# Kernel tuning notes

Hardware: AMD Instinct MI355X
Metric: run time of the kernel (lower is better)

## Reference

```python
import jax, jax.numpy as jnp
import numpy as np

N_NODES = 100000
N_EDGES = 1600000
NUM_FEATURES = 128
HIDDEN = 128


def _linear_init(key, fan_in, fan_out):
    kw, kb = jax.random.split(key)
    bound = 1.0 / np.sqrt(fan_in)
    w = jax.random.uniform(kw, (fan_in, fan_out), jnp.float32, -bound, bound)
    b = jax.random.uniform(kb, (fan_out,), jnp.float32, -bound, bound)
    return w, b


def setup_inputs() -> dict:
    key = jax.random.key(0)
    ks = jax.random.split(key, 8)
    x = jax.random.normal(ks[0], (N_NODES, NUM_FEATURES), jnp.float32)
    edge_index = jax.random.randint(ks[1], (2, N_EDGES), 0, N_NODES, jnp.int64)
    w11, b11 = _linear_init(ks[2], NUM_FEATURES, HIDDEN)
    w12, b12 = _linear_init(ks[3], HIDDEN, HIDDEN)
    w21, b21 = _linear_init(ks[4], HIDDEN, HIDDEN)
    w22, b22 = _linear_init(ks[5], HIDDEN, HIDDEN)
    w31, b31 = _linear_init(ks[6], HIDDEN, HIDDEN)
    w32, b32 = _linear_init(ks[7], HIDDEN, 1)
    return {"x": x, "edge_index": edge_index,
            "w11": w11, "b11": b11, "w12": w12, "b12": b12,
            "w21": w21, "b21": b21, "w22": w22, "b22": b22,
            "w31": w31, "b31": b31, "w32": w32, "b32": b32}


def _gin_conv(x, src, dst, w1, b1, w2, b2):
    # GINConv (eps=0): h_i = MLP(x_i + sum_{j->i} x_j)
    agg = jax.ops.segment_sum(x[src], dst, num_segments=N_NODES)
    h = x + agg
    h = jax.nn.relu(h @ w1 + b1)
    return h @ w2 + b2


def reference(x, edge_index, w11, b11, w12, b12, w21, b21, w22, b22, w31, b31, w32, b32):
    src, dst = edge_index[0], edge_index[1]
    h = _gin_conv(x, src, dst, w11, b11, w12, b12)
    h = _gin_conv(h, src, dst, w21, b21, w22, b22)
    h = _gin_conv(h, src, dst, w31, b31, w32, b32)  # [N, 1]
    return h
```

## Files before the change

kernel.cpp:

```cpp
#include <hip/hip_runtime.h>

#define NN 100000
#define NE 1600000
#define F 128
#define HALFN 50000
#define NBUCK ((NN + 255) >> 8)
#define SCAT_BLOCKS 512
#define EPB (NE / SCAT_BLOCKS)
#define TROWS 64
#define NTILE ((NN + TROWS - 1) / TROWS)
#define IDX_CAP 1536

typedef _Float16 f16x8 __attribute__((ext_vector_type(8)));
typedef float    f32x4 __attribute__((ext_vector_type(4)));
typedef unsigned short ushort8v __attribute__((ext_vector_type(8)));
typedef unsigned short ushort4v __attribute__((ext_vector_type(4)));

__device__ inline unsigned short f2h(float f) {
    _Float16 h = (_Float16)f;
    return __builtin_bit_cast(unsigned short, h);
}
__device__ inline float h2f(unsigned short u) {
    return (float)__builtin_bit_cast(_Float16, u);
}

__global__ __launch_bounds__(256) void k_bhist(const int* __restrict__ dst, int* __restrict__ bcnt) {
    __shared__ int sc[NBUCK];
    for (int i = threadIdx.x; i < NBUCK; i += 256) sc[i] = 0;
    __syncthreads();
    int stride = gridDim.x * 256;
    for (int e = blockIdx.x * 256 + threadIdx.x; e < NE; e += stride)
        atomicAdd(&sc[dst[e] >> 8], 1);
    __syncthreads();
    for (int i = threadIdx.x; i < NBUCK; i += 256) {
        int c = sc[i];
        if (c) atomicAdd(&bcnt[i], c);
    }
}

__global__ void k_bscan(const int* __restrict__ bcnt, int* __restrict__ bbase, int* __restrict__ bcur) {
    __shared__ int s[512];
    int t = threadIdx.x;
    int v = (t < NBUCK) ? bcnt[t] : 0;
    s[t] = v;
    __syncthreads();
    for (int off = 1; off < 512; off <<= 1) {
        int u = (t >= off) ? s[t - off] : 0;
        __syncthreads();
        s[t] += u;
        __syncthreads();
    }
    int excl = s[t] - v;
    if (t < NBUCK) { bbase[t] = excl; bcur[t] = excl; }
    if (t == 0) bbase[NBUCK] = NE;
}

__global__ __launch_bounds__(256) void k_scatterA(const int* __restrict__ src,
                                                  const int* __restrict__ dst,
                                                  int* __restrict__ bcur,
                                                  unsigned* __restrict__ scratch) {
    __shared__ uint2 sEdge[EPB];
    __shared__ int cnt[512];
    __shared__ int scn[512];
    __shared__ int cntB[512];
    __shared__ int gbase[512];
    __shared__ int ssum[256];

    const int tid = threadIdx.x;
    const int ebase = blockIdx.x * EPB;

#pragma unroll
    for (int i = tid; i < 512; i += 256) { cnt[i] = 0; cntB[i] = 0; }
    __syncthreads();

    for (int i = tid; i < EPB; i += 256) {
        int b = dst[ebase + i] >> 8;
        atomicAdd(&cnt[b], 1);
    }
    __syncthreads();

    int c0 = cnt[2 * tid], c1 = cnt[2 * tid + 1];
    ssum[tid] = c0 + c1;
    __syncthreads();
    for (int off = 1; off < 256; off <<= 1) {
        int v = (tid >= off) ? ssum[tid - off] : 0;
        __syncthreads();
        ssum[tid] += v;
        __syncthreads();
    }
    int texcl = (tid == 0) ? 0 : ssum[tid - 1];
    scn[2 * tid] = texcl;
    scn[2 * tid + 1] = texcl + c0;
#pragma unroll
    for (int i = tid; i < NBUCK; i += 256) {
        int c = cnt[i];
        gbase[i] = c ? atomicAdd(&bcur[i], c) : 0;
    }
    __syncthreads();

    for (int i = tid; i < EPB; i += 256) {
        int s = src[ebase + i], d = dst[ebase + i];
        int b = d >> 8;
        int rank = atomicAdd(&cntB[b], 1);
        sEdge[scn[b] + rank] = make_uint2((unsigned)s, (unsigned)d);
    }
    __syncthreads();

    for (int i = tid; i < EPB; i += 256) {
        uint2 ed = sEdge[i];
        int b = (int)(ed.y >> 8);
        unsigned w = ((ed.y & 255u) << 24) | ed.x;
        scratch[gbase[b] + (i - scn[b])] = w;
    }
}

__global__ __launch_bounds__(256) void k_fillB(const int* __restrict__ bbase,
                                               const unsigned* __restrict__ scratch,
                                               int* __restrict__ row_ptr,
                                               int* __restrict__ csr) {
    __shared__ int cnt[256];
    __shared__ int s[256];
    __shared__ int cur[256];
    int b = blockIdx.x;
    int base = bbase[b], end = bbase[b + 1];
    int t = threadIdx.x;
    cnt[t] = 0;
    __syncthreads();
    for (int i = base + t; i < end; i += 256)
        atomicAdd(&cnt[scratch[i] >> 24], 1);
    __syncthreads();
    int v = cnt[t];
    s[t] = v;
    __syncthreads();
    for (int off = 1; off < 256; off <<= 1) {
        int u = (t >= off) ? s[t - off] : 0;
        __syncthreads();
        s[t] += u;
        __syncthreads();
    }
    int excl = s[t] - v;
    int node = (b << 8) + t;
    if (node < NN) row_ptr[node] = base + excl;
    if (b == NBUCK - 1 && t == 0) row_ptr[NN] = NE;
    cur[t] = excl;
    __syncthreads();
    for (int i = base + t; i < end; i += 256) {
        unsigned w = scratch[i];
        int n = w >> 24;
        int p = atomicAdd(&cur[n], 1);
        csr[base + p] = (int)(w & 0xFFFFFFu);
    }
}

__global__ __launch_bounds__(256) void k_x2h(const float* __restrict__ x, unsigned short* __restrict__ xh) {
    int j = blockIdx.x * 256 + threadIdx.x;
    int c = blockIdx.y;
    if (j >= NN) return;
    const float4* px = (const float4*)&x[(size_t)j * F + c * 32];
    unsigned short* o = &xh[((size_t)c * NN + j) * 32];
#pragma unroll
    for (int half = 0; half < 4; ++half) {
        float4 v0 = px[half * 2], v1 = px[half * 2 + 1];
        ushort8v h;
        h[0] = f2h(v0.x); h[1] = f2h(v0.y); h[2] = f2h(v0.z); h[3] = f2h(v0.w);
        h[4] = f2h(v1.x); h[5] = f2h(v1.y); h[6] = f2h(v1.z); h[7] = f2h(v1.w);
        *(ushort8v*)(o + half * 8) = h;
    }
}

struct WPack {
    const float* w[5];
    unsigned short* t[5];
};

__global__ void k_w2h(WPack p) {
    int which = blockIdx.x >> 6;
    int idx = (blockIdx.x & 63) * 256 + threadIdx.x;
    int n = idx >> 7, k = idx & 127;
    p.t[which][idx] = f2h(p.w[which][k * 128 + n]);
}

template <bool LOC>
__device__ __forceinline__ void accum_half(float a[8], int st, int e,
                                           const int* __restrict__ sIdx,
                                           const int* __restrict__ gIdx,
                                           const unsigned short* __restrict__ Gc,
                                           int lofs, bool hb) {
    int p = st;
    for (; p + 4 <= e; p += 4) {
        int j0 = LOC ? sIdx[p]     : gIdx[p];
        int j1 = LOC ? sIdx[p + 1] : gIdx[p + 1];
        int j2 = LOC ? sIdx[p + 2] : gIdx[p + 2];
        int j3 = LOC ? sIdx[p + 3] : gIdx[p + 3];
        ushort8v v0 = {}, v1 = {}, v2 = {}, v3 = {};
        if ((j0 >= HALFN) == hb) v0 = *(const ushort8v*)&Gc[(size_t)j0 * 32 + lofs];
        if ((j1 >= HALFN) == hb) v1 = *(const ushort8v*)&Gc[(size_t)j1 * 32 + lofs];
        if ((j2 >= HALFN) == hb) v2 = *(const ushort8v*)&Gc[(size_t)j2 * 32 + lofs];
        if ((j3 >= HALFN) == hb) v3 = *(const ushort8v*)&Gc[(size_t)j3 * 32 + lofs];
#pragma unroll
        for (int k = 0; k < 8; ++k)
            a[k] += (h2f(v0[k]) + h2f(v1[k])) + (h2f(v2[k]) + h2f(v3[k]));
    }
    for (; p < e; ++p) {
        int j0 = LOC ? sIdx[p] : gIdx[p];
        if ((j0 >= HALFN) == hb) {
            ushort8v v0 = *(const ushort8v*)&Gc[(size_t)j0 * 32 + lofs];
#pragma unroll
            for (int k = 0; k < 8; ++k) a[k] += h2f(v0[k]);
        }
    }
}

__global__ __launch_bounds__(256, 8) void k_agg(const unsigned short* __restrict__ G,
                                                const int* __restrict__ row_ptr,
                                                const int* __restrict__ csr,
                                                unsigned short* __restrict__ PART) {
    __shared__ int sRP[TROWS + 1];
    __shared__ int sIdx[IDX_CAP];

    const int tid  = threadIdx.x;
    const int tile = blockIdx.x >> 3;
    const int cc   = blockIdx.x & 7;
    const int c    = cc & 3;
    const bool hb  = (cc >> 2) != 0;
    const int row0 = tile * TROWS;
    const unsigned short* Gc = G + (size_t)c * NN * 32;

    if (tid < TROWS + 1) {
        int n = row0 + tid;
        if (n > NN) n = NN;
        sRP[tid] = row_ptr[n];
    }
    __syncthreads();
    const int ibase = sRP[0];
    const int icnt  = sRP[TROWS] - ibase;
    const int icap  = icnt < IDX_CAP ? icnt : IDX_CAP;
    for (int i = tid; i < icap; i += 256) sIdx[i] = csr[ibase + i];
    __syncthreads();

    const int g    = tid >> 2;
    const int lofs = (tid & 3) * 8;
    const int node = row0 + g;
    if (node >= NN) return;

    float a[8] = {};
    if ((node >= HALFN) == hb) {
        ushort8v sh = *(const ushort8v*)&Gc[(size_t)node * 32 + lofs];
#pragma unroll
        for (int k = 0; k < 8; ++k) a[k] = h2f(sh[k]);
    }

    int st = sRP[g] - ibase, e = sRP[g + 1] - ibase;
    if (e <= icap)
        accum_half<true>(a, st, e, sIdx, csr + ibase, Gc, lofs, hb);
    else
        accum_half<false>(a, st, e, sIdx, csr + ibase, Gc, lofs, hb);

    ushort8v o;
#pragma unroll
    for (int k = 0; k < 8; ++k) o[k] = f2h(a[k]);
    *(ushort8v*)&PART[((size_t)cc * NN + node) * 32 + lofs] = o;
}

template <int L3>
__global__ __launch_bounds__(256, 6) void k_mlp(const unsigned short* __restrict__ PART,
                                                const unsigned short* __restrict__ W1,
                                                const float* __restrict__ b1,
                                                const unsigned short* __restrict__ W2,
                                                const float* __restrict__ b2,
                                                const float* __restrict__ w32,
                                                const float* __restrict__ b32,
                                                unsigned short* __restrict__ H,
                                                float* __restrict__ out) {
    __shared__ __align__(16) unsigned short sA[64 * 128];

    const int tid = threadIdx.x;
    const int row0 = blockIdx.x * 64;
    const int cg   = tid >> 6;
    const int lane = tid & 63;
    const int m16  = lane & 15;
    const int quad = lane >> 4;
    const size_t H1OFF = (size_t)4 * NN * 32;

#pragma unroll
    for (int i = 0; i < 4; ++i) {
        int unit = i * 256 + tid;
        int c    = unit >> 8;
        int idx  = unit & 255;
        int node = idx >> 2;
        int q    = idx & 3;
        ushort8v o = {};
        if (row0 + node < NN) {
            size_t base = ((size_t)c * NN + row0 + node) * 32 + q * 8;
            ushort8v v0 = *(const ushort8v*)&PART[base];
            ushort8v v1 = *(const ushort8v*)&PART[H1OFF + base];
#pragma unroll
            for (int k = 0; k < 8; ++k) o[k] = f2h(h2f(v0[k]) + h2f(v1[k]));
        }
        int u = c * 4 + q;
        *(ushort8v*)&sA[node * 128 + ((u ^ (node & 15)) << 3)] = o;
    }
    __syncthreads();

    f32x4 acc[4][2] = {};
#pragma unroll
    for (int ks = 0; ks < 4; ++ks) {
        f16x8 a[4];
#pragma unroll
        for (int rt = 0; rt < 4; ++rt) {
            int rowL = rt * 16 + m16;
            int u = ks * 4 + quad;
            a[rt] = *(const f16x8*)&sA[rowL * 128 + ((u ^ (rowL & 15)) << 3)];
        }
#pragma unroll
        for (int ct = 0; ct < 2; ++ct) {
            int widx = (cg * 32 + ct * 16 + m16) * 128 + ks * 32 + quad * 8;
            f16x8 b = *(const f16x8*)&W1[widx];
#pragma unroll
            for (int rt = 0; rt < 4; ++rt)
                acc[rt][ct] = __builtin_amdgcn_mfma_f32_16x16x32_f16(a[rt], b, acc[rt][ct], 0, 0, 0);
        }
    }

    if (L3) {
        float* psf = (float*)sA;
        __syncthreads();
#pragma unroll
        for (int rt = 0; rt < 4; ++rt) {
            float s[4] = {0.f, 0.f, 0.f, 0.f};
#pragma unroll
            for (int ct = 0; ct < 2; ++ct) {
                int col = cg * 32 + ct * 16 + m16;
                float bv = b1[col];
                float wv = w32[col];
#pragma unroll
                for (int i = 0; i < 4; ++i) {
                    float v = fmaxf(acc[rt][ct][i] + bv, 0.f);
                    s[i] += v * wv;
                }
            }
#pragma unroll
            for (int i = 0; i < 4; ++i) {
#pragma unroll
                for (int mask = 1; mask < 16; mask <<= 1)
                    s[i] += __shfl_xor(s[i], mask, 64);
            }
            if (m16 == 0) {
#pragma unroll
                for (int i = 0; i < 4; ++i) {
                    int rowL = rt * 16 + quad * 4 + i;
                    psf[rowL * 4 + cg] = s[i];
                }
            }
        }
        __syncthreads();
        if (tid < 64) {
            int row = row0 + tid;
            if (row < NN)
                out[row] = (psf[tid * 4] + psf[tid * 4 + 1]) + (psf[tid * 4 + 2] + psf[tid * 4 + 3]) + b32[0];
        }
        return;
    }

    __syncthreads();
#pragma unroll
    for (int rt = 0; rt < 4; ++rt) {
#pragma unroll
        for (int ct = 0; ct < 2; ++ct) {
            int col = cg * 32 + ct * 16 + m16;
            float bv = b1[col];
#pragma unroll
            for (int i = 0; i < 4; ++i) {
                int rL = rt * 16 + quad * 4 + i;
                float v = fmaxf(acc[rt][ct][i] + bv, 0.f);
                sA[rL * 128 + (((col >> 3) ^ (rL & 15)) << 3) + (col & 7)] = f2h(v);
            }
        }
    }
    __syncthreads();

    f32x4 acc2[4][2] = {};
#pragma unroll
    for (int ks = 0; ks < 4; ++ks) {
        f16x8 a[4];
#pragma unroll
        for (int rt = 0; rt < 4; ++rt) {
            int rowL = rt * 16 + m16;
            int u = ks * 4 + quad;
            a[rt] = *(const f16x8*)&sA[rowL * 128 + ((u ^ (rowL & 15)) << 3)];
        }
#pragma unroll
        for (int ct = 0; ct < 2; ++ct) {
            int widx = (cg * 32 + ct * 16 + m16) * 128 + ks * 32 + quad * 8;
            f16x8 b = *(const f16x8*)&W2[widx];
#pragma unroll
            for (int rt = 0; rt < 4; ++rt)
                acc2[rt][ct] = __builtin_amdgcn_mfma_f32_16x16x32_f16(a[rt], b, acc2[rt][ct], 0, 0, 0);
        }
    }

    __syncthreads();
#pragma unroll
    for (int rt = 0; rt < 4; ++rt) {
#pragma unroll
        for (int ct = 0; ct < 2; ++ct) {
            int col = cg * 32 + ct * 16 + m16;
            float bv = b2[col];
#pragma unroll
            for (int i = 0; i < 4; ++i) {
                int rL = rt * 16 + quad * 4 + i;
                float v = acc2[rt][ct][i] + bv;
                sA[rL * 128 + (((col >> 3) ^ (rL & 15)) << 3) + (col & 7)] = f2h(v);
            }
        }
    }
    __syncthreads();
    {
#pragma unroll
        for (int i = 0; i < 4; ++i) {
            int unit = i * 256 + tid;
            int c    = unit >> 8;
            int idx  = unit & 255;
            int node = idx >> 2;
            int q    = idx & 3;
            int u    = c * 4 + q;
            if (row0 + node < NN)
                *(ushort8v*)&H[((size_t)c * NN + row0 + node) * 32 + q * 8] =
                    *(const ushort8v*)&sA[node * 128 + ((u ^ (node & 15)) << 3)];
        }
    }
}

static inline size_t align256(size_t x) { return (x + 255) & ~(size_t)255; }

extern "C" void kernel_launch(void* const* d_in, const int* in_sizes, int n_in,
                              void* d_out, int out_size, void* d_ws, size_t ws_size,
                              hipStream_t stream) {
    const float* x   = (const float*)d_in[0];
    const int*   ei  = (const int*)d_in[1];
    const float* w11 = (const float*)d_in[2];
    const float* b11 = (const float*)d_in[3];
    const float* w12 = (const float*)d_in[4];
    const float* b12 = (const float*)d_in[5];
    const float* w21 = (const float*)d_in[6];
    const float* b21 = (const float*)d_in[7];
    const float* w22 = (const float*)d_in[8];
    const float* b22 = (const float*)d_in[9];
    const float* w31 = (const float*)d_in[10];
    const float* b31 = (const float*)d_in[11];
    const float* w32 = (const float*)d_in[12];
    const float* b32 = (const float*)d_in[13];
    float* out = (float*)d_out;

    const int* src = ei;
    const int* dst = ei + NE;

    char* ws = (char*)d_ws;
    size_t off = 0;
    unsigned short* Abuf = (unsigned short*)(ws + off); off += align256((size_t)NN * F * 2);
    unsigned short* Bbuf = (unsigned short*)(ws + off); off += align256((size_t)NN * F * 2);
    unsigned short* PART = (unsigned short*)(ws + off); off += align256((size_t)NN * F * 2 * 2);
    int* bcnt    = (int*)(ws + off); off += align256((size_t)NBUCK * 4);
    int* bbase   = (int*)(ws + off); off += align256((size_t)(NBUCK + 1) * 4);
    int* bcur    = (int*)(ws + off); off += align256((size_t)NBUCK * 4);
    int* row_ptr = (int*)(ws + off); off += align256((size_t)(NN + 1) * 4);
    int* csr     = (int*)(ws + off); off += align256((size_t)NE * 4);
    unsigned* scratch = (unsigned*)(ws + off); off += align256((size_t)NE * 4);
    unsigned short* wt[5];
    for (int i = 0; i < 5; ++i) {
        wt[i] = (unsigned short*)(ws + off); off += align256((size_t)128 * 128 * 2);
    }
    (void)ws_size;

    WPack wp;
    wp.w[0] = w11; wp.w[1] = w12; wp.w[2] = w21; wp.w[3] = w22; wp.w[4] = w31;
    for (int i = 0; i < 5; ++i) wp.t[i] = wt[i];
    k_w2h<<<320, 256, 0, stream>>>(wp);
    {
        dim3 gx((NN + 255) / 256, 4);
        k_x2h<<<gx, 256, 0, stream>>>(x, Abuf);
    }

    (void)hipMemsetAsync(bcnt, 0, (size_t)NBUCK * 4, stream);
    k_bhist<<<512, 256, 0, stream>>>(dst, bcnt);
    k_bscan<<<1, 512, 0, stream>>>(bcnt, bbase, bcur);
    k_scatterA<<<SCAT_BLOCKS, 256, 0, stream>>>(src, dst, bcur, scratch);
    k_fillB<<<NBUCK, 256, 0, stream>>>(bbase, scratch, row_ptr, csr);

    const int mlpTiles = (NN + 63) / 64;
    const int aggBlocks = NTILE * 8;

    k_agg<<<aggBlocks, 256, 0, stream>>>(Abuf, row_ptr, csr, PART);
    k_mlp<0><<<mlpTiles, 256, 0, stream>>>(PART, wt[0], b11, wt[1], b12,
                                           nullptr, nullptr, Bbuf, nullptr);
    k_agg<<<aggBlocks, 256, 0, stream>>>(Bbuf, row_ptr, csr, PART);
    k_mlp<0><<<mlpTiles, 256, 0, stream>>>(PART, wt[2], b21, wt[3], b22,
                                           nullptr, nullptr, Abuf, nullptr);
    k_agg<<<aggBlocks, 256, 0, stream>>>(Abuf, row_ptr, csr, PART);
    k_mlp<1><<<mlpTiles, 256, 0, stream>>>(PART, wt[4], b31, nullptr, nullptr,
                                           w32, b32, nullptr, out);
}
```

Measured before the change: 464.3 us.

## Partition CSR neighbor lists by source half so aggregation skips filtering

The CSR build now sorts each node's neighbor list into two groups, sources below and at-or-above the half-node boundary, and records a per-node split pointer. Each aggregation block, which handles one half of the source nodes, then walks only its own sub-range and loads neighbors unconditionally. Before, every block scanned the whole list and branched per index. This cuts the index reads and divergent predicated loads in the three aggregation passes. In exchange the CSR build does a bit more work and one extra row_split array is stored and read.

Result: faster. 432.9 us (-6.8%).

```diff
diff --git a/kernel.cpp b/kernel.cpp
--- a/kernel.cpp
+++ b/kernel.cpp
@@ -117,38 +117,49 @@
 __global__ __launch_bounds__(256) void k_fillB(const int* __restrict__ bbase,
                                                const unsigned* __restrict__ scratch,
                                                int* __restrict__ row_ptr,
+                                               int* __restrict__ row_split,
                                                int* __restrict__ csr) {
-    __shared__ int cnt[256];
-    __shared__ int s[256];
-    __shared__ int cur[256];
+    __shared__ int cnt[512];
+    __shared__ int cur[512];
+    __shared__ int ssum[256];
     int b = blockIdx.x;
     int base = bbase[b], end = bbase[b + 1];
     int t = threadIdx.x;
-    cnt[t] = 0;
-    __syncthreads();
-    for (int i = base + t; i < end; i += 256)
-        atomicAdd(&cnt[scratch[i] >> 24], 1);
-    __syncthreads();
-    int v = cnt[t];
-    s[t] = v;
-    __syncthreads();
-    for (int off = 1; off < 256; off <<= 1) {
-        int u = (t >= off) ? s[t - off] : 0;
-        __syncthreads();
-        s[t] += u;
-        __syncthreads();
-    }
-    int excl = s[t] - v;
-    int node = (b << 8) + t;
-    if (node < NN) row_ptr[node] = base + excl;
-    if (b == NBUCK - 1 && t == 0) row_ptr[NN] = NE;
-    cur[t] = excl;
+    cnt[t] = 0; cnt[t + 256] = 0;
     __syncthreads();
     for (int i = base + t; i < end; i += 256) {
         unsigned w = scratch[i];
         int n = w >> 24;
-        int p = atomicAdd(&cur[n], 1);
-        csr[base + p] = (int)(w & 0xFFFFFFu);
+        int h = (int)((w & 0xFFFFFFu) >= HALFN);
+        atomicAdd(&cnt[n * 2 + h], 1);
+    }
+    __syncthreads();
+    int c0 = cnt[2 * t], c1 = cnt[2 * t + 1];
+    ssum[t] = c0 + c1;
+    __syncthreads();
+    for (int off = 1; off < 256; off <<= 1) {
+        int u = (t >= off) ? ssum[t - off] : 0;
+        __syncthreads();
+        ssum[t] += u;
+        __syncthreads();
+    }
+    int texcl = (t == 0) ? 0 : ssum[t - 1];
+    int node = (b << 8) + t;
+    if (node < NN) {
+        row_ptr[node]   = base + texcl;
+        row_split[node] = base + texcl + c0;
+    }
+    if (b == NBUCK - 1 && t == 0) row_ptr[NN] = NE;
+    cur[2 * t] = texcl;
+    cur[2 * t + 1] = texcl + c0;
+    __syncthreads();
+    for (int i = base + t; i < end; i += 256) {
+        unsigned w = scratch[i];
+        int n = w >> 24;
+        int srcv = (int)(w & 0xFFFFFFu);
+        int h = (int)(srcv >= HALFN);
+        int p = atomicAdd(&cur[n * 2 + h], 1);
+        csr[base + p] = srcv;
     }
 }
 
@@ -181,48 +192,47 @@
 }
 
 template <bool LOC>
-__device__ __forceinline__ void accum_half(float a[8], int st, int e,
-                                           const int* __restrict__ sIdx,
-                                           const int* __restrict__ gIdx,
-                                           const unsigned short* __restrict__ Gc,
-                                           int lofs, bool hb) {
+__device__ __forceinline__ void accum1(float a[8], int st, int e,
+                                       const int* __restrict__ sIdx,
+                                       const int* __restrict__ gIdx,
+                                       const unsigned short* __restrict__ Gc,
+                                       int lofs) {
     int p = st;
     for (; p + 4 <= e; p += 4) {
         int j0 = LOC ? sIdx[p]     : gIdx[p];
         int j1 = LOC ? sIdx[p + 1] : gIdx[p + 1];
         int j2 = LOC ? sIdx[p + 2] : gIdx[p + 2];
         int j3 = LOC ? sIdx[p + 3] : gIdx[p + 3];
-        ushort8v v0 = {}, v1 = {}, v2 = {}, v3 = {};
-        if ((j0 >= HALFN) == hb) v0 = *(const ushort8v*)&Gc[(size_t)j0 * 32 + lofs];
-        if ((j1 >= HALFN) == hb) v1 = *(const ushort8v*)&Gc[(size_t)j1 * 32 + lofs];
-        if ((j2 >= HALFN) == hb) v2 = *(const ushort8v*)&Gc[(size_t)j2 * 32 + lofs];
-        if ((j3 >= HALFN) == hb) v3 = *(const ushort8v*)&Gc[(size_t)j3 * 32 + lofs];
+        ushort8v v0 = *(const ushort8v*)&Gc[(size_t)j0 * 32 + lofs];
+        ushort8v v1 = *(const ushort8v*)&Gc[(size_t)j1 * 32 + lofs];
+        ushort8v v2 = *(const ushort8v*)&Gc[(size_t)j2 * 32 + lofs];
+        ushort8v v3 = *(const ushort8v*)&Gc[(size_t)j3 * 32 + lofs];
 #pragma unroll
         for (int k = 0; k < 8; ++k)
             a[k] += (h2f(v0[k]) + h2f(v1[k])) + (h2f(v2[k]) + h2f(v3[k]));
     }
     for (; p < e; ++p) {
         int j0 = LOC ? sIdx[p] : gIdx[p];
-        if ((j0 >= HALFN) == hb) {
-            ushort8v v0 = *(const ushort8v*)&Gc[(size_t)j0 * 32 + lofs];
-#pragma unroll
-            for (int k = 0; k < 8; ++k) a[k] += h2f(v0[k]);
-        }
+        ushort8v v0 = *(const ushort8v*)&Gc[(size_t)j0 * 32 + lofs];
+#pragma unroll
+        for (int k = 0; k < 8; ++k) a[k] += h2f(v0[k]);
     }
 }
 
 __global__ __launch_bounds__(256, 8) void k_agg(const unsigned short* __restrict__ G,
                                                 const int* __restrict__ row_ptr,
+                                                const int* __restrict__ row_split,
                                                 const int* __restrict__ csr,
                                                 unsigned short* __restrict__ PART) {
     __shared__ int sRP[TROWS + 1];
+    __shared__ int sSP[TROWS];
     __shared__ int sIdx[IDX_CAP];
 
     const int tid  = threadIdx.x;
     const int tile = blockIdx.x >> 3;
     const int cc   = blockIdx.x & 7;
     const int c    = cc & 3;
-    const bool hb  = (cc >> 2) != 0;
+    const int hb   = cc >> 2;
     const int row0 = tile * TROWS;
     const unsigned short* Gc = G + (size_t)c * NN * 32;
 
@@ -230,6 +240,9 @@
         int n = row0 + tid;
         if (n > NN) n = NN;
         sRP[tid] = row_ptr[n];
+    } else if (tid >= 128 && tid < 128 + TROWS) {
+        int n = row0 + (tid - 128);
+        sSP[tid - 128] = (n < NN) ? row_split[n] : NE;
     }
     __syncthreads();
     const int ibase = sRP[0];
@@ -244,17 +257,19 @@
     if (node >= NN) return;
 
     float a[8] = {};
-    if ((node >= HALFN) == hb) {
+    if ((node >= HALFN) == (hb != 0)) {
         ushort8v sh = *(const ushort8v*)&Gc[(size_t)node * 32 + lofs];
 #pragma unroll
         for (int k = 0; k < 8; ++k) a[k] = h2f(sh[k]);
     }
 
-    int st = sRP[g] - ibase, e = sRP[g + 1] - ibase;
+    int st, e;
+    if (hb == 0) { st = sRP[g] - ibase; e = sSP[g] - ibase; }
+    else         { st = sSP[g] - ibase; e = sRP[g + 1] - ibase; }
     if (e <= icap)
-        accum_half<true>(a, st, e, sIdx, csr + ibase, Gc, lofs, hb);
+        accum1<true>(a, st, e, sIdx, csr + ibase, Gc, lofs);
     else
-        accum_half<false>(a, st, e, sIdx, csr + ibase, Gc, lofs, hb);
+        accum1<false>(a, st, e, sIdx, csr + ibase, Gc, lofs);
 
     ushort8v o;
 #pragma unroll
@@ -460,11 +475,12 @@
     unsigned short* Abuf = (unsigned short*)(ws + off); off += align256((size_t)NN * F * 2);
     unsigned short* Bbuf = (unsigned short*)(ws + off); off += align256((size_t)NN * F * 2);
     unsigned short* PART = (unsigned short*)(ws + off); off += align256((size_t)NN * F * 2 * 2);
-    int* bcnt    = (int*)(ws + off); off += align256((size_t)NBUCK * 4);
-    int* bbase   = (int*)(ws + off); off += align256((size_t)(NBUCK + 1) * 4);
-    int* bcur    = (int*)(ws + off); off += align256((size_t)NBUCK * 4);
-    int* row_ptr = (int*)(ws + off); off += align256((size_t)(NN + 1) * 4);
-    int* csr     = (int*)(ws + off); off += align256((size_t)NE * 4);
+    int* bcnt      = (int*)(ws + off); off += align256((size_t)NBUCK * 4);
+    int* bbase     = (int*)(ws + off); off += align256((size_t)(NBUCK + 1) * 4);
+    int* bcur      = (int*)(ws + off); off += align256((size_t)NBUCK * 4);
+    int* row_ptr   = (int*)(ws + off); off += align256((size_t)(NN + 1) * 4);
+    int* row_split = (int*)(ws + off); off += align256((size_t)NN * 4);
+    int* csr       = (int*)(ws + off); off += align256((size_t)NE * 4);
     unsigned* scratch = (unsigned*)(ws + off); off += align256((size_t)NE * 4);
     unsigned short* wt[5];
     for (int i = 0; i < 5; ++i) {
@@ -485,18 +501,18 @@
     k_bhist<<<512, 256, 0, stream>>>(dst, bcnt);
     k_bscan<<<1, 512, 0, stream>>>(bcnt, bbase, bcur);
     k_scatterA<<<SCAT_BLOCKS, 256, 0, stream>>>(src, dst, bcur, scratch);
-    k_fillB<<<NBUCK, 256, 0, stream>>>(bbase, scratch, row_ptr, csr);
+    k_fillB<<<NBUCK, 256, 0, stream>>>(bbase, scratch, row_ptr, row_split, csr);
 
     const int mlpTiles = (NN + 63) / 64;
     const int aggBlocks = NTILE * 8;
 
-    k_agg<<<aggBlocks, 256, 0, stream>>>(Abuf, row_ptr, csr, PART);
+    k_agg<<<aggBlocks, 256, 0, stream>>>(Abuf, row_ptr, row_split, csr, PART);
     k_mlp<0><<<mlpTiles, 256, 0, stream>>>(PART, wt[0], b11, wt[1], b12,
                                            nullptr, nullptr, Bbuf, nullptr);
-    k_agg<<<aggBlocks, 256, 0, stream>>>(Bbuf, row_ptr, csr, PART);
+    k_agg<<<aggBlocks, 256, 0, stream>>>(Bbuf, row_ptr, row_split, csr, PART);
     k_mlp<0><<<mlpTiles, 256, 0, stream>>>(PART, wt[2], b21, wt[3], b22,
                                            nullptr, nullptr, Abuf, nullptr);
-    k_agg<<<aggBlocks, 256, 0, stream>>>(Abuf, row_ptr, csr, PART);
+    k_agg<<<aggBlocks, 256, 0, stream>>>(Abuf, row_ptr, row_split, csr, PART);
     k_mlp<1><<<mlpTiles, 256, 0, stream>>>(PART, wt[4], b31, nullptr, nullptr,
                                            w32, b32, nullptr, out);
 }
```
